# Optimization experiments

Hardware: AMD Instinct MI355X
Metric: run time of the kernel (lower is better)

## Reference

```python
import jax, jax.numpy as jnp
import numpy as np

B = 32768
D_IN = 512
D_OUT = 512
N_DIGITS = 9
N_LEVELS = N_DIGITS + 1


def _xavier_uniform(key, shape, gain):
    # nn.init.xavier_uniform_ on Linear weight of shape (out, in)
    fan_out, fan_in = shape
    limit = gain * np.sqrt(6.0 / (fan_in + fan_out))
    return jax.random.uniform(key, shape, jnp.float32, -limit, limit)


def setup_inputs() -> dict:
    key = jax.random.key(0)
    kx, kv, *kw = jax.random.split(key, 2 + N_LEVELS)
    x = jax.random.normal(kx, (B, D_IN), dtype=jnp.float32)
    valuations = jax.random.randint(kv, (B,), 0, N_LEVELS, dtype=jnp.int64)
    # level-aware xavier init: gain = 1/(1 + 0.1*level)
    W = jnp.stack([
        _xavier_uniform(kw[l], (D_OUT, D_IN), 1.0 / (1.0 + 0.1 * l))
        for l in range(N_LEVELS)
    ], axis=0)  # (L, out, in)
    level_gates = jnp.ones((N_LEVELS,), dtype=jnp.float32)
    cross_level_attn = (jnp.eye(N_LEVELS, dtype=jnp.float32) * 0.9
                        + jnp.ones((N_LEVELS, N_LEVELS), dtype=jnp.float32) * 0.01)
    bias = jnp.zeros((D_OUT,), dtype=jnp.float32)
    return {"x": x, "valuations": valuations, "W": W,
            "level_gates": level_gates, "cross_level_attn": cross_level_attn,
            "bias": bias}


def reference(x, valuations, W, level_gates, cross_level_attn, bias):
    val = jnp.clip(valuations, 0, N_DIGITS)  # (B,)
    # 10 per-level linears as one batched GEMM: (B, L, out)
    level_outputs = jnp.einsum('bi,loi->blo', x, W)
    gates = jax.nn.sigmoid(level_gates)  # (L,)
    level_outputs = level_outputs * gates[None, :, None]
    # per-sample gather of own valuation level -> (B, out)
    output = jnp.take_along_axis(level_outputs, val[:, None, None], axis=1)[:, 0, :]
    # soft cross-level attention combine
    attn_weights = jax.nn.softmax(cross_level_attn[val], axis=-1)  # (B, L)
    weighted = jnp.einsum('bl,blo->bo', attn_weights, level_outputs)
    output = 0.7 * output + 0.3 * weighted
    return output + bias
```

## Files before the change

kernel.cpp:

```cpp
#include <hip/hip_runtime.h>

#define B_N 32768
#define D 512
#define DD (D * D)
#define NLEV 10
#define TM 128
#define TN 256
#define BK 32
#define NITER (D / BK)
#define NHB 128
#define MROWS_MAX 34048
#define MAX_RT (MROWS_MAX / TM)

typedef unsigned short u16;
typedef short s16x8 __attribute__((ext_vector_type(8)));
typedef u16 u16x8 __attribute__((ext_vector_type(8)));
typedef float f32x4 __attribute__((ext_vector_type(4)));

__device__ __forceinline__ u16 f2bf(float f) {
  union { float f; unsigned u; } v; v.f = f;
  unsigned r = v.u + 0x7fffu + ((v.u >> 16) & 1u);
  return (u16)(r >> 16);
}
__device__ __forceinline__ int clampv(int v) {
  return v < 0 ? 0 : (v > NLEV - 1 ? NLEV - 1 : v);
}

__global__ void k1(const float* __restrict__ W, const float* __restrict__ lg,
                   const float* __restrict__ attn, const int* __restrict__ val,
                   u16* __restrict__ weff, u16* __restrict__ hist,
                   int* __restrict__ perm) {
  const int t = threadIdx.x;
  if (blockIdx.x < DD / 256) {
    __shared__ float c[NLEV * NLEV];
    if (t < NLEV) {
      float g[NLEV], a[NLEV], mx = -1e30f;
      #pragma unroll
      for (int l = 0; l < NLEV; ++l) {
        g[l] = 1.0f / (1.0f + expf(-lg[l]));
        a[l] = attn[t * NLEV + l];
        mx = fmaxf(mx, a[l]);
      }
      float s = 0.f;
      #pragma unroll
      for (int l = 0; l < NLEV; ++l) { a[l] = expf(a[l] - mx); s += a[l]; }
      float inv = 1.0f / s;
      #pragma unroll
      for (int l = 0; l < NLEV; ++l) {
        float cc = 0.3f * a[l] * inv * g[l];
        if (l == t) cc += 0.7f * g[t];
        c[t * NLEV + l] = cc;
      }
    }
    __syncthreads();
    const int idx = blockIdx.x * 256 + t;
    float w[NLEV];
    #pragma unroll
    for (int l = 0; l < NLEV; ++l) w[l] = W[l * DD + idx];
    #pragma unroll
    for (int v = 0; v < NLEV; ++v) {
      float s = 0.f;
      #pragma unroll
      for (int l = 0; l < NLEV; ++l) s += c[v * NLEV + l] * w[l];
      weff[v * DD + idx] = f2bf(s);
    }
  } else {
    __shared__ int lc[NLEV];
    const int b = blockIdx.x - DD / 256;
    if (t < NLEV) lc[t] = 0;
    __syncthreads();
    const int gid = b * 256 + t;
    atomicAdd(&lc[clampv(val[gid])], 1);
    perm[gid] = -1;
    if (b < (MROWS_MAX - B_N) / 256) perm[B_N + b * 256 + t] = -1;
    __syncthreads();
    if (t < NLEV) hist[b * NLEV + t] = (u16)lc[t];
  }
}

__global__ void k2(const int* __restrict__ val, const u16* __restrict__ hist,
                   int* __restrict__ perm, int* __restrict__ starts) {
  __shared__ int h[NHB * NLEV];
  __shared__ int st[NLEV + 1];
  __shared__ int cnt[NLEV];
  __shared__ int lc[NLEV];
  const int t = threadIdx.x, b = blockIdx.x;
  for (int i = t; i < NHB * NLEV; i += 256) h[i] = hist[i];
  if (t < NLEV) lc[t] = 0;
  __syncthreads();
  if (t < NLEV) {
    int run = 0;
    for (int bb = 0; bb < NHB; ++bb) {
      int x = h[bb * NLEV + t];
      h[bb * NLEV + t] = run;
      run += x;
    }
    cnt[t] = run;
  }
  __syncthreads();
  if (t == 0) {
    int s = 0;
    for (int v = 0; v < NLEV; ++v) {
      st[v] = s;
      s += (cnt[v] + TM - 1) & ~(TM - 1);
    }
    st[NLEV] = s;
  }
  __syncthreads();
  const int gid = b * 256 + t;
  const int v = clampv(val[gid]);
  const int pos = atomicAdd(&lc[v], 1);
  perm[st[v] + h[b * NLEV + v] + pos] = gid;
  if (b == 0 && t <= NLEV) starts[t] = st[t];
}

__global__ __launch_bounds__(512, 4) void k3(
    const float* __restrict__ x, const u16* __restrict__ weff,
    const int* __restrict__ perm, const int* __restrict__ starts,
    const float* __restrict__ bias, float* __restrict__ out) {
  __shared__ u16 As[2][TM * BK];
  __shared__ u16 Bs[2][TN * BK];

  const int ct = blockIdx.x, rt = blockIdx.y;
  const int Mpad = starts[NLEV];
  if (rt * TM >= Mpad) return;

  int v = 0;
  #pragma unroll
  for (int i = 1; i < NLEV; ++i) if (rt * TM >= starts[i]) v = i;

  const int tid = threadIdx.x;
  const int lane = tid & 63, wave = tid >> 6;
  const int wm = (wave >> 2) * 64, wn = (wave & 3) * 64;
  const int fm = lane & 15;
  const int cb = lane >> 4;

  const int ar = tid >> 2;
  const int ah = tid & 3;
  int prow = perm[rt * TM + ar];
  if (prow < 0) prow = 0;
  const float* xrow = x + (size_t)prow * D + ah * 8;
  const int sw = (ar >> 1) & 3;
  const int aslot = ar * BK + ((ah ^ sw) << 3);

  const u16* wb = weff + ((size_t)v * D + ct * TN) * D;
  const int c0i = wave * 64 + lane;
  const int c1i = 512 + c0i;
  const int n0 = c0i >> 2, s0 = c0i & 3, kc0 = s0 ^ ((n0 >> 1) & 3);
  const int n1 = c1i >> 2, s1 = c1i & 3, kc1 = s1 ^ ((n1 >> 1) & 3);
  const u16* gb0 = wb + n0 * D + kc0 * 8;
  const u16* gb1 = wb + n1 * D + kc1 * 8;
  const int bdst0 = c0i * 8, bdst1 = c1i * 8;

  f32x4 acc[4][4];
  #pragma unroll
  for (int i = 0; i < 4; ++i)
    #pragma unroll
    for (int j = 0; j < 4; ++j) acc[i][j] = (f32x4){0.f, 0.f, 0.f, 0.f};

  {
    __builtin_amdgcn_global_load_lds(
        (const __attribute__((address_space(1))) void*)gb0,
        (__attribute__((address_space(3))) void*)(Bs[0] + bdst0), 16, 0, 0);
    __builtin_amdgcn_global_load_lds(
        (const __attribute__((address_space(1))) void*)gb1,
        (__attribute__((address_space(3))) void*)(Bs[0] + bdst1), 16, 0, 0);
    const f32x4* xp = (const f32x4*)xrow;
    f32x4 f0 = xp[0], f1 = xp[1];
    u16x8 cc;
    #pragma unroll
    for (int q = 0; q < 4; ++q) { cc[q] = f2bf(f0[q]); cc[4 + q] = f2bf(f1[q]); }
    *(u16x8*)(As[0] + aslot) = cc;
  }
  f32x4 cf0, cf1;
  {
    const f32x4* xp = (const f32x4*)(xrow + BK);
    cf0 = xp[0]; cf1 = xp[1];
  }
  __syncthreads();

  int p = 0;
  for (int i = 0; i < NITER; ++i) {
    const bool hn = (i + 1 < NITER);
    if (hn) {
      const int k1o = (i + 1) * BK;
      __builtin_amdgcn_global_load_lds(
          (const __attribute__((address_space(1))) void*)(gb0 + k1o),
          (__attribute__((address_space(3))) void*)(Bs[p ^ 1] + bdst0), 16, 0, 0);
      __builtin_amdgcn_global_load_lds(
          (const __attribute__((address_space(1))) void*)(gb1 + k1o),
          (__attribute__((address_space(3))) void*)(Bs[p ^ 1] + bdst1), 16, 0, 0);
    }
    f32x4 nf0, nf1;
    if (i + 2 < NITER) {
      const f32x4* xp = (const f32x4*)(xrow + (i + 2) * BK);
      nf0 = xp[0]; nf1 = xp[1];
    }
    s16x8 af[4], bf[4];
    #pragma unroll
    for (int t4 = 0; t4 < 4; ++t4) {
      const int m = wm + t4 * 16 + fm;
      af[t4] = *(const s16x8*)(As[p] + m * BK + ((cb ^ ((m >> 1) & 3)) << 3));
      const int n = wn + t4 * 16 + fm;
      bf[t4] = *(const s16x8*)(Bs[p] + n * BK + ((cb ^ ((n >> 1) & 3)) << 3));
    }
    #pragma unroll
    for (int tm = 0; tm < 4; ++tm)
      #pragma unroll
      for (int tn = 0; tn < 4; ++tn)
        acc[tm][tn] = __builtin_amdgcn_mfma_f32_16x16x32_bf16(af[tm], bf[tn], acc[tm][tn], 0, 0, 0);
    if (hn) {
      u16x8 cc;
      #pragma unroll
      for (int q = 0; q < 4; ++q) { cc[q] = f2bf(cf0[q]); cc[4 + q] = f2bf(cf1[q]); }
      *(u16x8*)(As[p ^ 1] + aslot) = cc;
      cf0 = nf0; cf1 = nf1;
    }
    __syncthreads();
    p ^= 1;
  }

  float bv[4];
  #pragma unroll
  for (int tn = 0; tn < 4; ++tn) bv[tn] = bias[ct * TN + wn + tn * 16 + fm];
  #pragma unroll
  for (int tm = 0; tm < 4; ++tm) {
    #pragma unroll
    for (int r = 0; r < 4; ++r) {
      const int mrow = wm + tm * 16 + (lane >> 4) * 4 + r;
      const int p2 = perm[rt * TM + mrow];
      if (p2 >= 0) {
        float* o = out + (size_t)p2 * D + ct * TN + wn + fm;
        #pragma unroll
        for (int tn = 0; tn < 4; ++tn)
          o[tn * 16] = acc[tm][tn][r] + bv[tn];
      }
    }
  }
}

extern "C" void kernel_launch(void* const* d_in, const int* in_sizes, int n_in,
                              void* d_out, int out_size, void* d_ws, size_t ws_size,
                              hipStream_t stream) {
  const float* x    = (const float*)d_in[0];
  const int*   val  = (const int*)d_in[1];
  const float* W    = (const float*)d_in[2];
  const float* lg   = (const float*)d_in[3];
  const float* attn = (const float*)d_in[4];
  const float* bias = (const float*)d_in[5];
  float* out = (float*)d_out;

  char* ws = (char*)d_ws;
  int* starts = (int*)(ws + 0);
  u16* hist   = (u16*)(ws + 64);
  int* perm   = (int*)(ws + 2688);
  u16* weff   = (u16*)(ws + 139264);

  k1<<<DD / 256 + NHB, 256, 0, stream>>>(W, lg, attn, val, weff, hist, perm);
  k2<<<NHB, 256, 0, stream>>>(val, hist, perm, starts);
  k3<<<dim3(D / TN, MAX_RT), 512, 0, stream>>>(x, weff, perm, starts, bias, out);
}
```

Before: 174.6 us.

## Make GEMM weight-stationary: keep full 128-col weight slab in LDS per level

Rewrites the main grouped GEMM so each block loads a whole 128x512 bf16 weight slab for one level into LDS (128 KB) and reuses it across many 64-row strips. Each wave streams its A rows straight from global memory into registers, with no LDS staging for A. A fixed grid of 4x64 blocks splits the sorted row space evenly, and group padding drops from 128 to 64 rows. The aim is to cut repeated weight traffic and padding waste, at the cost of occupancy (one block per CU because of the LDS footprint), uncoalesced per-lane A loads, and a barrier plus reload each time a block crosses into a new level.

```diff
diff --git a/kernel.cpp b/kernel.cpp
--- a/kernel.cpp
+++ b/kernel.cpp
@@ -4,13 +4,12 @@
 #define D 512
 #define DD (D * D)
 #define NLEV 10
-#define TM 128
-#define TN 256
-#define BK 32
-#define NITER (D / BK)
+#define ALIGN 64
 #define NHB 128
 #define MROWS_MAX 34048
-#define MAX_RT (MROWS_MAX / TM)
+#define TNB 128
+#define NCT (D / TNB)
+#define NRG 64
 
 typedef unsigned short u16;
 typedef short s16x8 __attribute__((ext_vector_type(8)));
@@ -102,7 +101,7 @@
     int s = 0;
     for (int v = 0; v < NLEV; ++v) {
       st[v] = s;
-      s += (cnt[v] + TM - 1) & ~(TM - 1);
+      s += (cnt[v] + ALIGN - 1) & ~(ALIGN - 1);
     }
     st[NLEV] = s;
   }
@@ -114,126 +113,122 @@
   if (b == 0 && t <= NLEV) starts[t] = st[t];
 }
 
-__global__ __launch_bounds__(512, 4) void k3(
+__global__ __launch_bounds__(512) void k3(
     const float* __restrict__ x, const u16* __restrict__ weff,
     const int* __restrict__ perm, const int* __restrict__ starts,
     const float* __restrict__ bias, float* __restrict__ out) {
-  __shared__ u16 As[2][TM * BK];
-  __shared__ u16 Bs[2][TN * BK];
-
-  const int ct = blockIdx.x, rt = blockIdx.y;
-  const int Mpad = starts[NLEV];
-  if (rt * TM >= Mpad) return;
-
-  int v = 0;
+  __shared__ u16 Bs[TNB * D];
+
+  const int ct = blockIdx.x;
+  const int rg = blockIdx.y;
+  const int tid = threadIdx.x;
+  const int lane = tid & 63, wv = tid >> 6;
+  const int fm = lane & 15, cb = lane >> 4;
+
+  int st[NLEV + 1];
   #pragma unroll
-  for (int i = 1; i < NLEV; ++i) if (rt * TM >= starts[i]) v = i;
-
-  const int tid = threadIdx.x;
-  const int lane = tid & 63, wave = tid >> 6;
-  const int wm = (wave >> 2) * 64, wn = (wave & 3) * 64;
-  const int fm = lane & 15;
-  const int cb = lane >> 4;
-
-  const int ar = tid >> 2;
-  const int ah = tid & 3;
-  int prow = perm[rt * TM + ar];
-  if (prow < 0) prow = 0;
-  const float* xrow = x + (size_t)prow * D + ah * 8;
-  const int sw = (ar >> 1) & 3;
-  const int aslot = ar * BK + ((ah ^ sw) << 3);
-
-  const u16* wb = weff + ((size_t)v * D + ct * TN) * D;
-  const int c0i = wave * 64 + lane;
-  const int c1i = 512 + c0i;
-  const int n0 = c0i >> 2, s0 = c0i & 3, kc0 = s0 ^ ((n0 >> 1) & 3);
-  const int n1 = c1i >> 2, s1 = c1i & 3, kc1 = s1 ^ ((n1 >> 1) & 3);
-  const u16* gb0 = wb + n0 * D + kc0 * 8;
-  const u16* gb1 = wb + n1 * D + kc1 * 8;
-  const int bdst0 = c0i * 8, bdst1 = c1i * 8;
-
-  f32x4 acc[4][4];
+  for (int i = 0; i <= NLEV; ++i) st[i] = starts[i];
+  const int Mpad = st[NLEV];
+  const int ts = Mpad >> 6;
+  const int q = ts >> 6, r = ts & 63;
+  const int s0 = rg < r ? rg * (q + 1) : r * (q + 1) + (rg - r) * q;
+  const int nst = rg < r ? q + 1 : q;
+  if (nst <= 0) return;
+  const int row0 = s0 << 6, row1 = (s0 + nst) << 6;
+
+  float bv[8];
   #pragma unroll
-  for (int i = 0; i < 4; ++i)
+  for (int nf = 0; nf < 8; ++nf) bv[nf] = bias[ct * TNB + nf * 16 + fm];
+
+  const u16* wct = weff + (size_t)ct * TNB * D;
+
+  for (int v = 0; v < NLEV; ++v) {
+    const int seg0 = row0 > st[v] ? row0 : st[v];
+    const int seg1 = row1 < st[v + 1] ? row1 : st[v + 1];
+    if (seg0 >= seg1) continue;
+
+    __syncthreads();
+    const u16* wb = wct + (size_t)v * DD;
     #pragma unroll
-    for (int j = 0; j < 4; ++j) acc[i][j] = (f32x4){0.f, 0.f, 0.f, 0.f};
-
-  {
-    __builtin_amdgcn_global_load_lds(
-        (const __attribute__((address_space(1))) void*)gb0,
-        (__attribute__((address_space(3))) void*)(Bs[0] + bdst0), 16, 0, 0);
-    __builtin_amdgcn_global_load_lds(
-        (const __attribute__((address_space(1))) void*)gb1,
-        (__attribute__((address_space(3))) void*)(Bs[0] + bdst1), 16, 0, 0);
-    const f32x4* xp = (const f32x4*)xrow;
-    f32x4 f0 = xp[0], f1 = xp[1];
-    u16x8 cc;
-    #pragma unroll
-    for (int q = 0; q < 4; ++q) { cc[q] = f2bf(f0[q]); cc[4 + q] = f2bf(f1[q]); }
-    *(u16x8*)(As[0] + aslot) = cc;
-  }
-  f32x4 cf0, cf1;
-  {
-    const f32x4* xp = (const f32x4*)(xrow + BK);
-    cf0 = xp[0]; cf1 = xp[1];
-  }
-  __syncthreads();
-
-  int p = 0;
-  for (int i = 0; i < NITER; ++i) {
-    const bool hn = (i + 1 < NITER);
-    if (hn) {
-      const int k1o = (i + 1) * BK;
+    for (int i = 0; i < 16; ++i) {
+      const int cid = i * 512 + tid;
+      const int n = cid >> 6, kc = cid & 63;
+      const int kcs = kc ^ (n & 7);
       __builtin_amdgcn_global_load_lds(
-          (const __attribute__((address_space(1))) void*)(gb0 + k1o),
-          (__attribute__((address_space(3))) void*)(Bs[p ^ 1] + bdst0), 16, 0, 0);
-      __builtin_amdgcn_global_load_lds(
-          (const __attribute__((address_space(1))) void*)(gb1 + k1o),
-          (__attribute__((address_space(3))) void*)(Bs[p ^ 1] + bdst1), 16, 0, 0);
-    }
-    f32x4 nf0, nf1;
-    if (i + 2 < NITER) {
-      const f32x4* xp = (const f32x4*)(xrow + (i + 2) * BK);
-      nf0 = xp[0]; nf1 = xp[1];
-    }
-    s16x8 af[4], bf[4];
-    #pragma unroll
-    for (int t4 = 0; t4 < 4; ++t4) {
-      const int m = wm + t4 * 16 + fm;
-      af[t4] = *(const s16x8*)(As[p] + m * BK + ((cb ^ ((m >> 1) & 3)) << 3));
-      const int n = wn + t4 * 16 + fm;
-      bf[t4] = *(const s16x8*)(Bs[p] + n * BK + ((cb ^ ((n >> 1) & 3)) << 3));
-    }
-    #pragma unroll
-    for (int tm = 0; tm < 4; ++tm)
-      #pragma unroll
-      for (int tn = 0; tn < 4; ++tn)
-        acc[tm][tn] = __builtin_amdgcn_mfma_f32_16x16x32_bf16(af[tm], bf[tn], acc[tm][tn], 0, 0, 0);
-    if (hn) {
-      u16x8 cc;
-      #pragma unroll
-      for (int q = 0; q < 4; ++q) { cc[q] = f2bf(cf0[q]); cc[4 + q] = f2bf(cf1[q]); }
-      *(u16x8*)(As[p ^ 1] + aslot) = cc;
-      cf0 = nf0; cf1 = nf1;
-    }
-    __syncthreads();
-    p ^= 1;
-  }
-
-  float bv[4];
-  #pragma unroll
-  for (int tn = 0; tn < 4; ++tn) bv[tn] = bias[ct * TN + wn + tn * 16 + fm];
-  #pragma unroll
-  for (int tm = 0; tm < 4; ++tm) {
-    #pragma unroll
-    for (int r = 0; r < 4; ++r) {
-      const int mrow = wm + tm * 16 + (lane >> 4) * 4 + r;
-      const int p2 = perm[rt * TM + mrow];
-      if (p2 >= 0) {
-        float* o = out + (size_t)p2 * D + ct * TN + wn + fm;
-        #pragma unroll
-        for (int tn = 0; tn < 4; ++tn)
-          o[tn * 16] = acc[tm][tn][r] + bv[tn];
+          (const __attribute__((address_space(1))) void*)(wb + n * D + kcs * 8),
+          (__attribute__((address_space(3))) void*)(Bs + cid * 8), 16, 0, 0);
+    }
+    __syncthreads();
+
+    const int ns = (seg1 - seg0) >> 6;
+    for (int si = wv; si < ns; si += 8) {
+      const int srow = seg0 + (si << 6);
+
+      const float* xb[4];
+      #pragma unroll
+      for (int m = 0; m < 4; ++m) {
+        const int p = perm[srow + m * 16 + fm];
+        xb[m] = x + (size_t)(p < 0 ? 0 : p) * D + cb * 8;
+      }
+
+      f32x4 acc[4][8];
+      #pragma unroll
+      for (int m = 0; m < 4; ++m)
+        #pragma unroll
+        for (int nf = 0; nf < 8; ++nf) acc[m][nf] = (f32x4){0.f, 0.f, 0.f, 0.f};
+
+      f32x4 p0[4], p1[4];
+      #pragma unroll
+      for (int m = 0; m < 4; ++m) {
+        const f32x4* qp = (const f32x4*)xb[m];
+        p0[m] = qp[0]; p1[m] = qp[1];
+      }
+
+      for (int k = 0; k < D / 32; ++k) {
+        s16x8 af[4];
+        #pragma unroll
+        for (int m = 0; m < 4; ++m) {
+          u16x8 cc;
+          #pragma unroll
+          for (int qq = 0; qq < 4; ++qq) {
+            cc[qq] = f2bf(p0[m][qq]); cc[4 + qq] = f2bf(p1[m][qq]);
+          }
+          af[m] = (s16x8)cc;
+        }
+        if (k < D / 32 - 1) {
+          #pragma unroll
+          for (int m = 0; m < 4; ++m) {
+            const f32x4* qp = (const f32x4*)(xb[m] + (k + 1) * 32);
+            p0[m] = qp[0]; p1[m] = qp[1];
+          }
+        }
+        s16x8 bf[8];
+        #pragma unroll
+        for (int nf = 0; nf < 8; ++nf) {
+          const int n = nf * 16 + fm;
+          const int chunk = (n << 6) + ((k * 4 + cb) ^ (fm & 7));
+          bf[nf] = *(const s16x8*)(Bs + chunk * 8);
+        }
+        #pragma unroll
+        for (int m = 0; m < 4; ++m)
+          #pragma unroll
+          for (int nf = 0; nf < 8; ++nf)
+            acc[m][nf] = __builtin_amdgcn_mfma_f32_16x16x32_bf16(
+                af[m], bf[nf], acc[m][nf], 0, 0, 0);
+      }
+
+      #pragma unroll
+      for (int m = 0; m < 4; ++m) {
+        #pragma unroll
+        for (int rr = 0; rr < 4; ++rr) {
+          const int p2 = perm[srow + m * 16 + cb * 4 + rr];
+          if (p2 >= 0) {
+            float* o = out + (size_t)p2 * D + ct * TNB + fm;
+            #pragma unroll
+            for (int nf = 0; nf < 8; ++nf)
+              o[nf * 16] = acc[m][nf][rr] + bv[nf];
+          }
+        }
       }
     }
   }
@@ -258,5 +253,5 @@
 
   k1<<<DD / 256 + NHB, 256, 0, stream>>>(W, lg, attn, val, weff, hist, perm);
   k2<<<NHB, 256, 0, stream>>>(val, hist, perm, starts);
-  k3<<<dim3(D / TN, MAX_RT), 512, 0, stream>>>(x, weff, perm, starts, bias, out);
-}
+  k3<<<dim3(NCT, NRG), 512, 0, stream>>>(x, weff, perm, starts, bias, out);
+}
```

Measured after the change: 191.1 us. 1.09x slower.

## Triple-buffer B tiles with two-stage-ahead async loads and explicit waitcnt barriers

Applied to the files above, without the earlier changes.

Changes the GEMM main loop from double to triple buffering for the weight tile. Direct global-to-LDS loads are issued two K-steps ahead, and __syncthreads is replaced by manual vmcnt/lgkmcnt waits so the newest prefetch can stay in flight across the barrier. It also raises wave priority around the MFMA block. The aim is to hide global load latency better, at the cost of 50% more LDS per block, which may reduce occupancy. The vmcnt(4) count also assumes a particular order in which the x loads and the LDS loads are issued.

```diff
diff --git a/kernel.cpp b/kernel.cpp
--- a/kernel.cpp
+++ b/kernel.cpp
@@ -118,8 +118,8 @@
     const float* __restrict__ x, const u16* __restrict__ weff,
     const int* __restrict__ perm, const int* __restrict__ starts,
     const float* __restrict__ bias, float* __restrict__ out) {
-  __shared__ u16 As[2][TM * BK];
-  __shared__ u16 Bs[2][TN * BK];
+  __shared__ u16 As[3][TM * BK];
+  __shared__ u16 Bs[3][TN * BK];
 
   const int ct = blockIdx.x, rt = blockIdx.y;
   const int Mpad = starts[NLEV];
@@ -159,12 +159,6 @@
     for (int j = 0; j < 4; ++j) acc[i][j] = (f32x4){0.f, 0.f, 0.f, 0.f};
 
   {
-    __builtin_amdgcn_global_load_lds(
-        (const __attribute__((address_space(1))) void*)gb0,
-        (__attribute__((address_space(3))) void*)(Bs[0] + bdst0), 16, 0, 0);
-    __builtin_amdgcn_global_load_lds(
-        (const __attribute__((address_space(1))) void*)gb1,
-        (__attribute__((address_space(3))) void*)(Bs[0] + bdst1), 16, 0, 0);
     const f32x4* xp = (const f32x4*)xrow;
     f32x4 f0 = xp[0], f1 = xp[1];
     u16x8 cc;
@@ -177,47 +171,73 @@
     const f32x4* xp = (const f32x4*)(xrow + BK);
     cf0 = xp[0]; cf1 = xp[1];
   }
-  __syncthreads();
-
-  int p = 0;
+  __builtin_amdgcn_global_load_lds(
+      (const __attribute__((address_space(1))) void*)gb0,
+      (__attribute__((address_space(3))) void*)(Bs[0] + bdst0), 16, 0, 0);
+  __builtin_amdgcn_global_load_lds(
+      (const __attribute__((address_space(1))) void*)gb1,
+      (__attribute__((address_space(3))) void*)(Bs[0] + bdst1), 16, 0, 0);
+  __builtin_amdgcn_global_load_lds(
+      (const __attribute__((address_space(1))) void*)(gb0 + BK),
+      (__attribute__((address_space(3))) void*)(Bs[1] + bdst0), 16, 0, 0);
+  __builtin_amdgcn_global_load_lds(
+      (const __attribute__((address_space(1))) void*)(gb1 + BK),
+      (__attribute__((address_space(3))) void*)(Bs[1] + bdst1), 16, 0, 0);
+  asm volatile("s_waitcnt vmcnt(0)" ::: "memory");
+  asm volatile("s_waitcnt lgkmcnt(0)" ::: "memory");
+  __builtin_amdgcn_s_barrier();
+  __builtin_amdgcn_sched_barrier(0);
+
+  u16 *Ar = (u16*)As[0], *Aw = (u16*)As[1], *Ax = (u16*)As[2];
+  u16 *Br = (u16*)Bs[0], *Bm = (u16*)Bs[1], *Bw = (u16*)Bs[2];
+
   for (int i = 0; i < NITER; ++i) {
+    const bool h2 = (i + 2 < NITER);
     const bool hn = (i + 1 < NITER);
-    if (hn) {
-      const int k1o = (i + 1) * BK;
-      __builtin_amdgcn_global_load_lds(
-          (const __attribute__((address_space(1))) void*)(gb0 + k1o),
-          (__attribute__((address_space(3))) void*)(Bs[p ^ 1] + bdst0), 16, 0, 0);
-      __builtin_amdgcn_global_load_lds(
-          (const __attribute__((address_space(1))) void*)(gb1 + k1o),
-          (__attribute__((address_space(3))) void*)(Bs[p ^ 1] + bdst1), 16, 0, 0);
-    }
     f32x4 nf0, nf1;
-    if (i + 2 < NITER) {
+    if (h2) {
       const f32x4* xp = (const f32x4*)(xrow + (i + 2) * BK);
       nf0 = xp[0]; nf1 = xp[1];
     }
+    if (h2) {
+      const int ko = (i + 2) * BK;
+      __builtin_amdgcn_global_load_lds(
+          (const __attribute__((address_space(1))) void*)(gb0 + ko),
+          (__attribute__((address_space(3))) void*)(Bw + bdst0), 16, 0, 0);
+      __builtin_amdgcn_global_load_lds(
+          (const __attribute__((address_space(1))) void*)(gb1 + ko),
+          (__attribute__((address_space(3))) void*)(Bw + bdst1), 16, 0, 0);
+    }
     s16x8 af[4], bf[4];
     #pragma unroll
     for (int t4 = 0; t4 < 4; ++t4) {
       const int m = wm + t4 * 16 + fm;
-      af[t4] = *(const s16x8*)(As[p] + m * BK + ((cb ^ ((m >> 1) & 3)) << 3));
+      af[t4] = *(const s16x8*)(Ar + m * BK + ((cb ^ ((m >> 1) & 3)) << 3));
       const int n = wn + t4 * 16 + fm;
-      bf[t4] = *(const s16x8*)(Bs[p] + n * BK + ((cb ^ ((n >> 1) & 3)) << 3));
-    }
+      bf[t4] = *(const s16x8*)(Br + n * BK + ((cb ^ ((n >> 1) & 3)) << 3));
+    }
+    __builtin_amdgcn_s_setprio(1);
     #pragma unroll
     for (int tm = 0; tm < 4; ++tm)
       #pragma unroll
       for (int tn = 0; tn < 4; ++tn)
         acc[tm][tn] = __builtin_amdgcn_mfma_f32_16x16x32_bf16(af[tm], bf[tn], acc[tm][tn], 0, 0, 0);
+    __builtin_amdgcn_s_setprio(0);
     if (hn) {
       u16x8 cc;
       #pragma unroll
       for (int q = 0; q < 4; ++q) { cc[q] = f2bf(cf0[q]); cc[4 + q] = f2bf(cf1[q]); }
-      *(u16x8*)(As[p ^ 1] + aslot) = cc;
-      cf0 = nf0; cf1 = nf1;
-    }
-    __syncthreads();
-    p ^= 1;
+      *(u16x8*)(Aw + aslot) = cc;
+      if (h2) { cf0 = nf0; cf1 = nf1; }
+      if (h2) asm volatile("s_waitcnt vmcnt(4)" ::: "memory");
+      else    asm volatile("s_waitcnt vmcnt(0)" ::: "memory");
+      asm volatile("s_waitcnt lgkmcnt(0)" ::: "memory");
+      __builtin_amdgcn_s_barrier();
+      __builtin_amdgcn_sched_barrier(0);
+      u16* t;
+      t = Ar; Ar = Aw; Aw = Ax; Ax = t;
+      t = Br; Br = Bm; Bm = Bw; Bw = t;
+    }
   }
 
   float bv[4];
```

After: 171.8 us. No clear change (-1.6%).

## Replace LDS-tiled GEMM with register-direct 32-row tiles spanning full output width

Applied to the files above, without the earlier changes.

The grouped GEMM kernel drops its shared-memory double buffering. Each wave now loads its A (x rows, converted to bf16) and B (weff) MFMA fragments straight from global memory into registers, with one-step register prefetch. Each block covers 32 rows across all 512 output columns, and per-level padding shrinks from 128 to 64 rows, so less padded work is wasted. The cost is losing LDS reuse: every wave re-reads the same x rows and each block re-reads 512x512 weights from global/L2, which raises cache traffic.

```diff
diff --git a/kernel.cpp b/kernel.cpp
--- a/kernel.cpp
+++ b/kernel.cpp
@@ -4,13 +4,11 @@
 #define D 512
 #define DD (D * D)
 #define NLEV 10
-#define TM 128
-#define TN 256
-#define BK 32
-#define NITER (D / BK)
+#define PAD 64
 #define NHB 128
 #define MROWS_MAX 34048
-#define MAX_RT (MROWS_MAX / TM)
+#define WM 32
+#define NMT (MROWS_MAX / WM)
 
 typedef unsigned short u16;
 typedef short s16x8 __attribute__((ext_vector_type(8)));
@@ -102,7 +100,7 @@
     int s = 0;
     for (int v = 0; v < NLEV; ++v) {
       st[v] = s;
-      s += (cnt[v] + TM - 1) & ~(TM - 1);
+      s += (cnt[v] + PAD - 1) & ~(PAD - 1);
     }
     st[NLEV] = s;
   }
@@ -118,122 +116,89 @@
     const float* __restrict__ x, const u16* __restrict__ weff,
     const int* __restrict__ perm, const int* __restrict__ starts,
     const float* __restrict__ bias, float* __restrict__ out) {
-  __shared__ u16 As[2][TM * BK];
-  __shared__ u16 Bs[2][TN * BK];
-
-  const int ct = blockIdx.x, rt = blockIdx.y;
+  const int mt = blockIdx.x;
+  const int rbase = mt * WM;
   const int Mpad = starts[NLEV];
-  if (rt * TM >= Mpad) return;
+  if (rbase >= Mpad) return;
 
   int v = 0;
   #pragma unroll
-  for (int i = 1; i < NLEV; ++i) if (rt * TM >= starts[i]) v = i;
+  for (int i = 1; i < NLEV; ++i) if (rbase >= starts[i]) v = i;
 
   const int tid = threadIdx.x;
-  const int lane = tid & 63, wave = tid >> 6;
-  const int wm = (wave >> 2) * 64, wn = (wave & 3) * 64;
-  const int fm = lane & 15;
-  const int cb = lane >> 4;
-
-  const int ar = tid >> 2;
-  const int ah = tid & 3;
-  int prow = perm[rt * TM + ar];
-  if (prow < 0) prow = 0;
-  const float* xrow = x + (size_t)prow * D + ah * 8;
-  const int sw = (ar >> 1) & 3;
-  const int aslot = ar * BK + ((ah ^ sw) << 3);
-
-  const u16* wb = weff + ((size_t)v * D + ct * TN) * D;
-  const int c0i = wave * 64 + lane;
-  const int c1i = 512 + c0i;
-  const int n0 = c0i >> 2, s0 = c0i & 3, kc0 = s0 ^ ((n0 >> 1) & 3);
-  const int n1 = c1i >> 2, s1 = c1i & 3, kc1 = s1 ^ ((n1 >> 1) & 3);
-  const u16* gb0 = wb + n0 * D + kc0 * 8;
-  const u16* gb1 = wb + n1 * D + kc1 * 8;
-  const int bdst0 = c0i * 8, bdst1 = c1i * 8;
-
-  f32x4 acc[4][4];
-  #pragma unroll
-  for (int i = 0; i < 4; ++i)
-    #pragma unroll
-    for (int j = 0; j < 4; ++j) acc[i][j] = (f32x4){0.f, 0.f, 0.f, 0.f};
-
+  const int lane = tid & 63, wvi = tid >> 6;
+  const int fm = lane & 15, cbk = lane >> 4;
+  const int wn = wvi * 64;
+
+  const int pr0 = perm[rbase + fm];
+  const int pr1 = perm[rbase + 16 + fm];
+  const float* a0 = x + (size_t)(pr0 < 0 ? 0 : pr0) * D + cbk * 8;
+  const float* a1 = x + (size_t)(pr1 < 0 ? 0 : pr1) * D + cbk * 8;
+  const u16* wb = weff + (size_t)v * DD + (size_t)(wn + fm) * D + cbk * 8;
+
+  f32x4 acc[2][4];
+  #pragma unroll
+  for (int m = 0; m < 2; ++m)
+    #pragma unroll
+    for (int n = 0; n < 4; ++n) acc[m][n] = (f32x4){0.f, 0.f, 0.f, 0.f};
+
+  f32x4 pa00, pa01, pa10, pa11;
+  s16x8 pb0, pb1, pb2, pb3;
   {
-    __builtin_amdgcn_global_load_lds(
-        (const __attribute__((address_space(1))) void*)gb0,
-        (__attribute__((address_space(3))) void*)(Bs[0] + bdst0), 16, 0, 0);
-    __builtin_amdgcn_global_load_lds(
-        (const __attribute__((address_space(1))) void*)gb1,
-        (__attribute__((address_space(3))) void*)(Bs[0] + bdst1), 16, 0, 0);
-    const f32x4* xp = (const f32x4*)xrow;
-    f32x4 f0 = xp[0], f1 = xp[1];
-    u16x8 cc;
-    #pragma unroll
-    for (int q = 0; q < 4; ++q) { cc[q] = f2bf(f0[q]); cc[4 + q] = f2bf(f1[q]); }
-    *(u16x8*)(As[0] + aslot) = cc;
-  }
-  f32x4 cf0, cf1;
-  {
-    const f32x4* xp = (const f32x4*)(xrow + BK);
-    cf0 = xp[0]; cf1 = xp[1];
-  }
-  __syncthreads();
-
-  int p = 0;
-  for (int i = 0; i < NITER; ++i) {
-    const bool hn = (i + 1 < NITER);
-    if (hn) {
-      const int k1o = (i + 1) * BK;
-      __builtin_amdgcn_global_load_lds(
-          (const __attribute__((address_space(1))) void*)(gb0 + k1o),
-          (__attribute__((address_space(3))) void*)(Bs[p ^ 1] + bdst0), 16, 0, 0);
-      __builtin_amdgcn_global_load_lds(
-          (const __attribute__((address_space(1))) void*)(gb1 + k1o),
-          (__attribute__((address_space(3))) void*)(Bs[p ^ 1] + bdst1), 16, 0, 0);
-    }
-    f32x4 nf0, nf1;
-    if (i + 2 < NITER) {
-      const f32x4* xp = (const f32x4*)(xrow + (i + 2) * BK);
-      nf0 = xp[0]; nf1 = xp[1];
-    }
-    s16x8 af[4], bf[4];
-    #pragma unroll
-    for (int t4 = 0; t4 < 4; ++t4) {
-      const int m = wm + t4 * 16 + fm;
-      af[t4] = *(const s16x8*)(As[p] + m * BK + ((cb ^ ((m >> 1) & 3)) << 3));
-      const int n = wn + t4 * 16 + fm;
-      bf[t4] = *(const s16x8*)(Bs[p] + n * BK + ((cb ^ ((n >> 1) & 3)) << 3));
-    }
-    #pragma unroll
-    for (int tm = 0; tm < 4; ++tm)
-      #pragma unroll
-      for (int tn = 0; tn < 4; ++tn)
-        acc[tm][tn] = __builtin_amdgcn_mfma_f32_16x16x32_bf16(af[tm], bf[tn], acc[tm][tn], 0, 0, 0);
-    if (hn) {
-      u16x8 cc;
-      #pragma unroll
-      for (int q = 0; q < 4; ++q) { cc[q] = f2bf(cf0[q]); cc[4 + q] = f2bf(cf1[q]); }
-      *(u16x8*)(As[p ^ 1] + aslot) = cc;
-      cf0 = nf0; cf1 = nf1;
-    }
-    __syncthreads();
-    p ^= 1;
+    const f32x4* A0 = (const f32x4*)a0;
+    const f32x4* A1 = (const f32x4*)a1;
+    pa00 = A0[0]; pa01 = A0[1];
+    pa10 = A1[0]; pa11 = A1[1];
+    pb0 = *(const s16x8*)(wb);
+    pb1 = *(const s16x8*)(wb + 16 * D);
+    pb2 = *(const s16x8*)(wb + 32 * D);
+    pb3 = *(const s16x8*)(wb + 48 * D);
+  }
+
+  #pragma unroll
+  for (int k = 0; k < D / 32; ++k) {
+    u16x8 t0, t1;
+    #pragma unroll
+    for (int q = 0; q < 4; ++q) {
+      t0[q] = f2bf(pa00[q]); t0[4 + q] = f2bf(pa01[q]);
+      t1[q] = f2bf(pa10[q]); t1[4 + q] = f2bf(pa11[q]);
+    }
+    const s16x8 ca0 = (s16x8)t0, ca1 = (s16x8)t1;
+    const s16x8 cb0 = pb0, cb1 = pb1, cb2 = pb2, cb3 = pb3;
+    if (k + 1 < D / 32) {
+      const int off = (k + 1) * 32;
+      const f32x4* A0 = (const f32x4*)(a0 + off);
+      const f32x4* A1 = (const f32x4*)(a1 + off);
+      pa00 = A0[0]; pa01 = A0[1];
+      pa10 = A1[0]; pa11 = A1[1];
+      pb0 = *(const s16x8*)(wb + off);
+      pb1 = *(const s16x8*)(wb + 16 * D + off);
+      pb2 = *(const s16x8*)(wb + 32 * D + off);
+      pb3 = *(const s16x8*)(wb + 48 * D + off);
+    }
+    acc[0][0] = __builtin_amdgcn_mfma_f32_16x16x32_bf16(ca0, cb0, acc[0][0], 0, 0, 0);
+    acc[0][1] = __builtin_amdgcn_mfma_f32_16x16x32_bf16(ca0, cb1, acc[0][1], 0, 0, 0);
+    acc[0][2] = __builtin_amdgcn_mfma_f32_16x16x32_bf16(ca0, cb2, acc[0][2], 0, 0, 0);
+    acc[0][3] = __builtin_amdgcn_mfma_f32_16x16x32_bf16(ca0, cb3, acc[0][3], 0, 0, 0);
+    acc[1][0] = __builtin_amdgcn_mfma_f32_16x16x32_bf16(ca1, cb0, acc[1][0], 0, 0, 0);
+    acc[1][1] = __builtin_amdgcn_mfma_f32_16x16x32_bf16(ca1, cb1, acc[1][1], 0, 0, 0);
+    acc[1][2] = __builtin_amdgcn_mfma_f32_16x16x32_bf16(ca1, cb2, acc[1][2], 0, 0, 0);
+    acc[1][3] = __builtin_amdgcn_mfma_f32_16x16x32_bf16(ca1, cb3, acc[1][3], 0, 0, 0);
   }
 
   float bv[4];
   #pragma unroll
-  for (int tn = 0; tn < 4; ++tn) bv[tn] = bias[ct * TN + wn + tn * 16 + fm];
-  #pragma unroll
-  for (int tm = 0; tm < 4; ++tm) {
+  for (int tn = 0; tn < 4; ++tn) bv[tn] = bias[wn + tn * 16 + fm];
+  #pragma unroll
+  for (int m = 0; m < 2; ++m) {
     #pragma unroll
     for (int r = 0; r < 4; ++r) {
-      const int mrow = wm + tm * 16 + (lane >> 4) * 4 + r;
-      const int p2 = perm[rt * TM + mrow];
+      const int p2 = perm[rbase + m * 16 + cbk * 4 + r];
       if (p2 >= 0) {
-        float* o = out + (size_t)p2 * D + ct * TN + wn + fm;
+        float* o = out + (size_t)p2 * D + wn + fm;
         #pragma unroll
         for (int tn = 0; tn < 4; ++tn)
-          o[tn * 16] = acc[tm][tn][r] + bv[tn];
+          o[tn * 16] = acc[m][tn][r] + bv[tn];
       }
     }
   }
@@ -258,5 +223,5 @@
 
   k1<<<DD / 256 + NHB, 256, 0, stream>>>(W, lg, attn, val, weff, hist, perm);
   k2<<<NHB, 256, 0, stream>>>(val, hist, perm, starts);
-  k3<<<dim3(D / TN, MAX_RT), 512, 0, stream>>>(x, weff, perm, starts, bias, out);
-}
+  k3<<<NMT, 512, 0, stream>>>(x, weff, perm, starts, bias, out);
+}
```

After: 263.2 us. +50.8%, slower.
